# Performance work log

Measured on AMD Instinct MI355X. Metric: run time of the kernel, lower is better.

Reference implementation:

```python
import jax, jax.numpy as jnp
import numpy as np
import math

D = 2048  # hidden_size
B, S = 4, 2048
EPS = 1e-5


def _ln(z, g, b):
    m = jnp.mean(z, axis=-1, keepdims=True)
    v = jnp.mean(jnp.square(z - m), axis=-1, keepdims=True)
    return (z - m) * jax.lax.rsqrt(v + EPS) * g + b


def _rotate_half(x):
    h = x.shape[-1] // 2
    return jnp.concatenate([-x[..., h:], x[..., :h]], axis=-1)


def _mas_normalize(logits):
    m = jnp.max(jnp.abs(logits), axis=-1, keepdims=True)
    return logits / (m + 1e-9)


def setup_inputs() -> dict:
    key = jax.random.key(0)
    ks = jax.random.split(key, 12)
    std = 0.02
    return {
        "x": jax.random.normal(ks[0], (B, S, D), dtype=jnp.float32),
        "position_ids": jnp.arange(S, dtype=jnp.int32),
        "ln1_g": jnp.ones((D,), jnp.float32),
        "ln1_b": jnp.zeros((D,), jnp.float32),
        # stacked params for [q, k, v, o]
        "mu_w": std * jax.random.normal(ks[1], (4, D, D), dtype=jnp.float32),
        "mu_b": jnp.zeros((4, D), jnp.float32),
        "proto_w": std * jax.random.normal(ks[2], (4, D, D), dtype=jnp.float32),
        "gate": jnp.zeros((4, D), jnp.float32),
        "pt_w": std * jax.random.normal(ks[3], (4, D, D), dtype=jnp.float32),
        "pln_g": jnp.ones((4, D), jnp.float32),
        "pln_b": jnp.zeros((4, D), jnp.float32),
        "incoming": std * jax.random.normal(ks[4], (4, D, D), dtype=jnp.float32),
    }


def reference(x, position_ids, ln1_g, ln1_b, mu_w, mu_b, proto_w, gate,
              pt_w, pln_g, pln_b, incoming):
    d = x.shape[-1]
    inv_sqrt_d = 1.0 / math.sqrt(d)

    # proto_state = proto_weight + LN(Linear(incoming))  per module [4, D, D]
    prc = jnp.einsum('nij,noj->nio', incoming, pt_w)
    proto_state = proto_w + _ln(prc, pln_g[:, None, :], pln_b[:, None, :])

    ln1_out = _ln(x, ln1_g, ln1_b)            # [B,S,D]
    ctx = jnp.mean(ln1_out, axis=1)           # [B,D]

    # qkv computation outputs: silu(ln1_out @ mu_w.T + mu_b) for n in {q,k,v}
    comp = jax.nn.silu(jnp.einsum('bsd,nod->nbso', ln1_out, mu_w[:3])
                       + mu_b[:3][:, None, None, :])            # [3,B,S,D]
    # routing from context vector
    match_ctx = jnp.einsum('bd,nod->nbo', ctx, proto_state[:3]) * inv_sqrt_d
    routing = match_ctx + gate[:3][:, None, :]                  # [3,B,D]
    gating = _mas_normalize(routing)
    masked = gating[:, :, None, :] * comp                       # [3,B,S,D]
    q, k, v = masked[0], masked[1], masked[2]

    # RoPE over full hidden dim (num_heads == 1)
    seq = position_ids.shape[0]
    inv_freq = 1.0 / (10000.0 ** (jnp.arange(0, d, 2, dtype=jnp.float32) / d))
    t = jnp.arange(seq, dtype=jnp.float32)
    freqs = t[:, None] * inv_freq[None, :]
    emb = jnp.concatenate([freqs, freqs], axis=-1)              # [S,D]
    cos = jnp.cos(emb)[position_ids]
    sin = jnp.sin(emb)[position_ids]
    q = q * cos + _rotate_half(q) * sin
    k = k * cos + _rotate_half(k) * sin

    # causal single-head attention, scale 1/sqrt(head_dim=D)
    scores = jnp.einsum('bqd,bkd->bqk', q, k) * inv_sqrt_d      # [B,S,S]
    causal = jnp.tril(jnp.ones((seq, seq), dtype=bool))
    scores = jnp.where(causal, scores, jnp.finfo(scores.dtype).min)
    probs = jax.nn.softmax(scores, axis=-1)
    attn_out = jnp.einsum('bqk,bkd->bqd', probs, v)             # [B,S,D]

    # output SPL + routing
    ctx_o = jnp.mean(attn_out, axis=1)
    c_o = jax.nn.silu(jnp.einsum('bsd,od->bso', attn_out, mu_w[3]) + mu_b[3])
    match_o = jnp.einsum('bd,od->bo', ctx_o, proto_state[3]) * inv_sqrt_d
    gating_o = _mas_normalize(match_o + gate[3])
    x_out = x + gating_o[:, None, :] * c_o
    return x_out
```

## Files before the change

### kernel.cpp

```cpp
#include <hip/hip_runtime.h>
#include <hip/hip_bf16.h>

#define Dh 2048
#define Bh 4
#define Sh 2048
#define NROW 8192
#define HALF 1024
#define INV_SQRT_D 0.022097086912079608f
#define LNEPS 1e-5f

typedef __hip_bfloat16 bf16;
typedef short short8 __attribute__((ext_vector_type(8)));
typedef float f32x4 __attribute__((ext_vector_type(4)));

__device__ inline float warp_sum(float x) {
#pragma unroll
  for (int o = 32; o > 0; o >>= 1) x += __shfl_down(x, o);
  return x;
}
__device__ inline float warp_max(float x) {
#pragma unroll
  for (int o = 32; o > 0; o >>= 1) x = fmaxf(x, __shfl_down(x, o));
  return x;
}
__device__ inline float block_sum(float x, float* sm4) {
  x = warp_sum(x);
  int w = threadIdx.x >> 6;
  if ((threadIdx.x & 63) == 0) sm4[w] = x;
  __syncthreads();
  float r = sm4[0] + sm4[1] + sm4[2] + sm4[3];
  __syncthreads();
  return r;
}
__device__ inline float block_max(float x, float* sm4) {
  x = warp_max(x);
  int w = threadIdx.x >> 6;
  if ((threadIdx.x & 63) == 0) sm4[w] = x;
  __syncthreads();
  float r = fmaxf(fmaxf(sm4[0], sm4[1]), fmaxf(sm4[2], sm4[3]));
  __syncthreads();
  return r;
}

__device__ inline void gload_lds16(const void* g, void* lds) {
  __builtin_amdgcn_global_load_lds(
      (const __attribute__((address_space(1))) unsigned int*)(unsigned long long)g,
      (__attribute__((address_space(3))) unsigned int*)(unsigned long long)lds,
      16, 0, 0);
}

#define MM(R, AF)                                                              \
  acc[R][0] = __builtin_amdgcn_mfma_f32_16x16x32_bf16(AF, b0, acc[R][0], 0, 0, 0); \
  acc[R][1] = __builtin_amdgcn_mfma_f32_16x16x32_bf16(AF, b1, acc[R][1], 0, 0, 0); \
  acc[R][2] = __builtin_amdgcn_mfma_f32_16x16x32_bf16(AF, b2, acc[R][2], 0, 0, 0); \
  acc[R][3] = __builtin_amdgcn_mfma_f32_16x16x32_bf16(AF, b3, acc[R][3], 0, 0, 0);

template <int MODE>
__global__ __launch_bounds__(512) void pgemm(
    const bf16* __restrict__ Aall, const bf16* __restrict__ Ball,
    void* __restrict__ Call, int N, int K, int lda, int ldb,
    long sAz, long sBz, long sCz,
    const float* __restrict__ e0, const float* __restrict__ e1,
    const float* __restrict__ e2) {
  const int bm0 = blockIdx.x * 256;
  const int bn0 = blockIdx.y * 256;
  if (MODE == 2 && bn0 > bm0 + 255) return;
  const int z = blockIdx.z;
  const bf16* A = Aall + (long)z * sAz;
  const bf16* B = Ball + (long)z * sBz;

  __shared__ __align__(16) char smem[65536];
  const int tid = threadIdx.x;
  const int l = tid & 63, w = tid >> 6;
  const int wr = w >> 2, wc = w & 3;

  f32x4 acc[8][4] = {};
  const int nt = K >> 5;

  const int sg = (((l & 3) ^ ((l >> 3) & 3)) << 3);
  const int srow = (w << 4) + (l >> 2);
  const bf16* aS0 = A + (long)(bm0 + srow) * lda + sg;
  const bf16* aS1 = A + (long)(bm0 + 128 + srow) * lda + sg;
  const bf16* bS0 = B + (long)(bn0 + srow) * ldb + sg;
  const bf16* bS1 = B + (long)(bn0 + 128 + srow) * ldb + sg;
  char* const dA = smem + (w << 10);
  char* const dB = smem + 16384 + (w << 10);

  auto stageA = [&](int tt) {
    int boff = (tt & 1) << 15;
    gload_lds16(aS0 + (tt << 5), dA + boff);
    gload_lds16(aS1 + (tt << 5), dA + boff + 8192);
  };
  auto stageB = [&](int tt) {
    int boff = (tt & 1) << 15;
    gload_lds16(bS0 + (tt << 5), dB + boff);
    gload_lds16(bS1 + (tt << 5), dB + boff + 8192);
  };

  stageA(0); stageB(0);
  if (nt > 1) stageB(1);
  if (nt > 1) asm volatile("s_waitcnt vmcnt(2)" ::: "memory");
  else        asm volatile("s_waitcnt vmcnt(0)" ::: "memory");
  __builtin_amdgcn_sched_barrier(0);
  asm volatile("s_barrier" ::: "memory");

  const int rslot = (((l >> 4) ^ ((l >> 1) & 3)) << 4);
  const int abyte = (((wr << 7) + (l & 15)) << 6) + rslot;
  const int bbyte = (((wc << 6) + (l & 15)) << 6) + rslot;

  for (int t = 0; t < nt; ++t) {
    const char* Ab = smem + ((t & 1) << 15);
    const char* Bb = Ab + 16384;
    short8 b0 = *(const short8*)(Bb + bbyte);
    short8 b1 = *(const short8*)(Bb + bbyte + 1024);
    short8 b2 = *(const short8*)(Bb + bbyte + 2048);
    short8 b3 = *(const short8*)(Bb + bbyte + 3072);
    short8 a0 = *(const short8*)(Ab + abyte);
    short8 a1 = *(const short8*)(Ab + abyte + 1024);
    short8 a2 = *(const short8*)(Ab + abyte + 2048);
    short8 a3 = *(const short8*)(Ab + abyte + 3072);
    if (t + 1 < nt) stageA(t + 1);
    MM(0, a0) MM(1, a1) MM(2, a2) MM(3, a3)
    asm volatile("s_waitcnt lgkmcnt(0)" ::: "memory");
    asm volatile("s_barrier" ::: "memory");
    short8 a4 = *(const short8*)(Ab + abyte + 4096);
    short8 a5 = *(const short8*)(Ab + abyte + 5120);
    short8 a6 = *(const short8*)(Ab + abyte + 6144);
    short8 a7 = *(const short8*)(Ab + abyte + 7168);
    if (t + 2 < nt) stageB(t + 2);
    MM(4, a4) MM(5, a5) MM(6, a6) MM(7, a7)
    if (t < nt - 1) {
      asm volatile("s_waitcnt lgkmcnt(0)" ::: "memory");
      if (t + 2 < nt) asm volatile("s_waitcnt vmcnt(2)" ::: "memory");
      else            asm volatile("s_waitcnt vmcnt(0)" ::: "memory");
      __builtin_amdgcn_sched_barrier(0);
      asm volatile("s_barrier" ::: "memory");
    }
  }

  const int lc = l & 15, lr4 = (l >> 4) << 2;
#pragma unroll
  for (int fr = 0; fr < 8; ++fr) {
    int gr0 = bm0 + (wr << 7) + fr * 16 + lr4;
#pragma unroll
    for (int fc = 0; fc < 4; ++fc) {
      int gc = bn0 + (wc << 6) + fc * 16 + lc;
#pragma unroll
      for (int qv = 0; qv < 4; ++qv) {
        int gr = gr0 + qv;
        float a = acc[fr][fc][qv];
        if (MODE == 0) {
          ((float*)Call + (long)z * sCz)[(long)gr * N + gc] = a;
        } else if (MODE == 1) {
          float val = a + e0[z * Dh + gc];
          float sil = val / (1.f + __expf(-val));
          int bb = gr >> 11;
          float g = e1[(z * Bh + bb) * Dh + gc];
          ((bf16*)Call + (long)z * sCz)[(long)gr * N + gc] =
              __float2bfloat16(sil * g);
        } else if (MODE == 2) {
          ((float*)Call + (long)z * sCz)[(long)gr * N + gc] = a * INV_SQRT_D;
        } else {
          float val = a + e0[gc];
          float sil = val / (1.f + __expf(-val));
          int bb = gr >> 11;
          ((float*)Call)[(long)gr * N + gc] =
              e2[(long)gr * N + gc] + e1[bb * Dh + gc] * sil;
        }
      }
    }
  }
}

__global__ __launch_bounds__(512) void pgemm_h(
    const bf16* __restrict__ Aall, const bf16* __restrict__ Ball,
    bf16* __restrict__ Call, int N, int lda, int ldb,
    long sAz, long sBz, long sCz) {
  const int fid = blockIdx.x;
  const int p = fid >> 8, q = fid & 255;
  const int mh = q >> 5;
  const int z = (q >> 3) & 3, ni = q & 7;
  const int mi = p ? (15 - mh) : mh;
  const int bm0 = mi * 128, bn0 = ni * 256;
  const bf16* A = Aall + (long)z * sAz;
  const bf16* B = Ball + (long)z * sBz;

  __shared__ __align__(16) char smem[49152];
  const int tid = threadIdx.x;
  const int l = tid & 63, w = tid >> 6;
  const int wr = w >> 2, wc = w & 3;
  f32x4 acc[4][4] = {};
  const int nt = (bm0 + 128) >> 5;

  const int sg = (((l & 3) ^ ((l >> 3) & 3)) << 3);
  const int srow = (w << 4) + (l >> 2);
  const bf16* aS = A + (long)(bm0 + srow) * lda + sg;
  const bf16* bS0 = B + (long)(bn0 + srow) * ldb + sg;
  const bf16* bS1 = B + (long)(bn0 + 128 + srow) * ldb + sg;
  char* const dA = smem + (w << 10);
  char* const dB = smem + 8192 + (w << 10);

  auto stageA = [&](int tt) {
    gload_lds16(aS + (tt << 5), dA + (tt & 1) * 24576);
  };
  auto stageB = [&](int tt) {
    int boff = (tt & 1) * 24576;
    gload_lds16(bS0 + (tt << 5), dB + boff);
    gload_lds16(bS1 + (tt << 5), dB + boff + 8192);
  };

  stageA(0); stageB(0);
  if (nt > 1) stageB(1);
  if (nt > 1) asm volatile("s_waitcnt vmcnt(2)" ::: "memory");
  else        asm volatile("s_waitcnt vmcnt(0)" ::: "memory");
  __builtin_amdgcn_sched_barrier(0);
  asm volatile("s_barrier" ::: "memory");

  const int rslot = (((l >> 4) ^ ((l >> 1) & 3)) << 4);
  const int abyte = (((wr << 6) + (l & 15)) << 6) + rslot;
  const int bbyte = (((wc << 6) + (l & 15)) << 6) + rslot;

  for (int t = 0; t < nt; ++t) {
    const char* Ab = smem + (t & 1) * 24576;
    const char* Bb = Ab + 8192;
    short8 b0 = *(const short8*)(Bb + bbyte);
    short8 b1 = *(const short8*)(Bb + bbyte + 1024);
    short8 b2 = *(const short8*)(Bb + bbyte + 2048);
    short8 b3 = *(const short8*)(Bb + bbyte + 3072);
    short8 a0 = *(const short8*)(Ab + abyte);
    short8 a1 = *(const short8*)(Ab + abyte + 1024);
    if (t + 1 < nt) stageA(t + 1);
    MM(0, a0) MM(1, a1)
    asm volatile("s_waitcnt lgkmcnt(0)" ::: "memory");
    asm volatile("s_barrier" ::: "memory");
    short8 a2 = *(const short8*)(Ab + abyte + 2048);
    short8 a3 = *(const short8*)(Ab + abyte + 3072);
    if (t + 2 < nt) stageB(t + 2);
    MM(2, a2) MM(3, a3)
    if (t < nt - 1) {
      asm volatile("s_waitcnt lgkmcnt(0)" ::: "memory");
      if (t + 2 < nt) asm volatile("s_waitcnt vmcnt(2)" ::: "memory");
      else            asm volatile("s_waitcnt vmcnt(0)" ::: "memory");
      __builtin_amdgcn_sched_barrier(0);
      asm volatile("s_barrier" ::: "memory");
    }
  }

  const int lc = l & 15, lr4 = (l >> 4) << 2;
  bf16* C = Call + (long)z * sCz;
#pragma unroll
  for (int fr = 0; fr < 4; ++fr) {
    int gr0 = bm0 + (wr << 6) + fr * 16 + lr4;
#pragma unroll
    for (int fc = 0; fc < 4; ++fc) {
      int gc = bn0 + (wc << 6) + fc * 16 + lc;
#pragma unroll
      for (int qv = 0; qv < 4; ++qv) {
        C[(long)(gr0 + qv) * N + gc] = __float2bfloat16(acc[fr][fc][qv]);
      }
    }
  }
}

__global__ __launch_bounds__(256) void cvt3_kernel(
    const float* __restrict__ s0, const float* __restrict__ s1,
    const float* __restrict__ s2, bf16* __restrict__ o0, bf16* __restrict__ o1,
    bf16* __restrict__ o2, long n) {
  const float* in = (blockIdx.y == 0) ? s0 : (blockIdx.y == 1) ? s1 : s2;
  bf16* out = (blockIdx.y == 0) ? o0 : (blockIdx.y == 1) ? o1 : o2;
  long i = ((long)blockIdx.x * 256 + threadIdx.x) * 4;
  if (i >= n) return;
  float4 v = *(const float4*)(in + i);
  out[i + 0] = __float2bfloat16(v.x);
  out[i + 1] = __float2bfloat16(v.y);
  out[i + 2] = __float2bfloat16(v.z);
  out[i + 3] = __float2bfloat16(v.w);
}

__global__ __launch_bounds__(256) void transpose_kernel(const bf16* __restrict__ in,
                                                        bf16* __restrict__ out) {
  __shared__ bf16 t[64][65];
  int b = blockIdx.z;
  int s0 = blockIdx.x * 64, d0 = blockIdx.y * 64;
  const bf16* ib = in + (long)b * Sh * Dh;
  bf16* ob = out + (long)b * Sh * Dh;
  int tx = threadIdx.x & 63, ty = threadIdx.x >> 6;
#pragma unroll
  for (int r = ty; r < 64; r += 4) t[r][tx] = ib[(long)(s0 + r) * Dh + d0 + tx];
  __syncthreads();
#pragma unroll
  for (int r = ty; r < 64; r += 4) ob[(long)(d0 + r) * Sh + s0 + tx] = t[tx][r];
}

__global__ __launch_bounds__(256) void ln1_kernel(const float* __restrict__ x,
    const float* __restrict__ g, const float* __restrict__ b, bf16* __restrict__ out) {
  __shared__ float sm4[4];
  long r = blockIdx.x;
  const float* row = x + r * Dh;
  float v[8];
  float s = 0.f, s2 = 0.f;
#pragma unroll
  for (int c = 0; c < 8; ++c) {
    float t = row[threadIdx.x + c * 256];
    v[c] = t; s += t; s2 += t * t;
  }
  s = block_sum(s, sm4);
  s2 = block_sum(s2, sm4);
  float mean = s * (1.f / Dh);
  float rstd = rsqrtf(s2 * (1.f / Dh) - mean * mean + LNEPS);
#pragma unroll
  for (int c = 0; c < 8; ++c) {
    int o = threadIdx.x + c * 256;
    out[r * Dh + o] = __float2bfloat16((v[c] - mean) * rstd * g[o] + b[o]);
  }
}

__global__ __launch_bounds__(256) void meanrow_kernel(const bf16* __restrict__ in,
                                                      float* __restrict__ outbd) {
  int gid = blockIdx.x * 256 + threadIdx.x;
  int s0 = blockIdx.y * 128;
  long base = ((long)(gid >> 11) * Sh + s0) * Dh + (gid & 2047);
  float s = 0.f;
  for (int t = 0; t < 128; ++t) s += __bfloat162float(in[base + (long)t * Dh]);
  atomicAdd(&outbd[gid], s * (1.f / Sh));
}

__global__ __launch_bounds__(256) void route_kernel(
    const float* __restrict__ prc, const float* __restrict__ proto_w,
    const float* __restrict__ pln_g, const float* __restrict__ pln_b,
    const float* __restrict__ gate, const float* __restrict__ ctx,
    float* __restrict__ routing, float* __restrict__ ps3) {
  __shared__ float sm4[4];
  int i = blockIdx.x, n = blockIdx.y;
  long rb = ((long)n * Dh + i) * Dh;
  float v[8];
  float s = 0.f, s2 = 0.f;
#pragma unroll
  for (int c = 0; c < 8; ++c) {
    float t = prc[rb + threadIdx.x + c * 256];
    v[c] = t; s += t; s2 += t * t;
  }
  s = block_sum(s, sm4);
  s2 = block_sum(s2, sm4);
  float mean = s * (1.f / Dh);
  float rstd = rsqrtf(s2 * (1.f / Dh) - mean * mean + LNEPS);
  if (n == 3) {
#pragma unroll
    for (int c = 0; c < 8; ++c) {
      int o = threadIdx.x + c * 256;
      float ps = proto_w[rb + o] + (v[c] - mean) * rstd * pln_g[3 * Dh + o] + pln_b[3 * Dh + o];
      ps3[(long)i * Dh + o] = ps;
    }
  } else {
    float acc[4] = {0.f, 0.f, 0.f, 0.f};
#pragma unroll
    for (int c = 0; c < 8; ++c) {
      int o = threadIdx.x + c * 256;
      float ps = proto_w[rb + o] + (v[c] - mean) * rstd * pln_g[n * Dh + o] + pln_b[n * Dh + o];
#pragma unroll
      for (int b = 0; b < 4; ++b) acc[b] += ps * ctx[b * Dh + o];
    }
    for (int b = 0; b < 4; ++b) {
      float r = block_sum(acc[b], sm4);
      if (threadIdx.x == 0)
        routing[(n * 4 + b) * Dh + i] = r * INV_SQRT_D + gate[n * Dh + i];
    }
  }
}

__global__ __launch_bounds__(256) void route_o_kernel(
    const float* __restrict__ ps3, const float* __restrict__ ctxo,
    const float* __restrict__ gate, float* __restrict__ routing) {
  __shared__ float sm4[4];
  int i = blockIdx.x;
  float acc[4] = {0.f, 0.f, 0.f, 0.f};
#pragma unroll
  for (int c = 0; c < 8; ++c) {
    int o = threadIdx.x + c * 256;
    float p = ps3[(long)i * Dh + o];
#pragma unroll
    for (int b = 0; b < 4; ++b) acc[b] += p * ctxo[b * Dh + o];
  }
  for (int b = 0; b < 4; ++b) {
    float r = block_sum(acc[b], sm4);
    if (threadIdx.x == 0)
      routing[(12 + b) * Dh + i] = r * INV_SQRT_D + gate[3 * Dh + i];
  }
}

__global__ __launch_bounds__(256) void masnorm_kernel(const float* __restrict__ rin,
                                                      float* __restrict__ gout) {
  __shared__ float sm4[4];
  long r = blockIdx.x;
  float m = 0.f;
#pragma unroll
  for (int c = 0; c < 8; ++c)
    m = fmaxf(m, fabsf(rin[r * Dh + threadIdx.x + c * 256]));
  m = block_max(m, sm4);
  float inv = 1.f / (m + 1e-9f);
#pragma unroll
  for (int c = 0; c < 8; ++c) {
    int o = threadIdx.x + c * 256;
    gout[r * Dh + o] = rin[r * Dh + o] * inv;
  }
}

__global__ __launch_bounds__(256) void rope_table_kernel(float* __restrict__ cosT,
                                                         float* __restrict__ sinT) {
  int idx = blockIdx.x * 256 + threadIdx.x;
  int t = idx >> 10, f = idx & 1023;
  float inv_freq = expf(-(float)f * (9.210340371976184f / 1024.f));
  float ang = (float)t * inv_freq;
  cosT[idx] = cosf(ang);
  sinT[idx] = sinf(ang);
}

__global__ __launch_bounds__(256) void rope_kernel(bf16* __restrict__ q, bf16* __restrict__ k,
    const int* __restrict__ pos, const float* __restrict__ cosT,
    const float* __restrict__ sinT) {
  long r = blockIdx.x;
  int s = (int)(r & (Sh - 1));
  int p = pos[s];
#pragma unroll
  for (int c = 0; c < 4; ++c) {
    int t = threadIdx.x + c * 256;
    float cv = cosT[(long)p * HALF + t];
    float sv = sinT[(long)p * HALF + t];
    long i1 = r * Dh + t, i2 = i1 + HALF;
    float q1 = __bfloat162float(q[i1]), q2 = __bfloat162float(q[i2]);
    q[i1] = __float2bfloat16(q1 * cv - q2 * sv);
    q[i2] = __float2bfloat16(q2 * cv + q1 * sv);
    float k1 = __bfloat162float(k[i1]), k2 = __bfloat162float(k[i2]);
    k[i1] = __float2bfloat16(k1 * cv - k2 * sv);
    k[i2] = __float2bfloat16(k2 * cv + k1 * sv);
  }
}

__global__ __launch_bounds__(256) void softmax_kernel(const float* __restrict__ scores,
                                                      bf16* __restrict__ probs) {
  __shared__ float buf[Sh];
  __shared__ float sm4[4];
  long r = blockIdx.x;
  int qi = (int)(r & (Sh - 1));
  const float* row = scores + r * (long)Sh;
  bf16* prow = probs + r * (long)Sh;
  int n = qi + 1;
  float m = -3.0e38f;
  for (int o = threadIdx.x; o < n; o += 256) {
    float x = row[o]; buf[o] = x; m = fmaxf(m, x);
  }
  m = block_max(m, sm4);
  float s = 0.f;
  for (int o = threadIdx.x; o < n; o += 256) {
    float e = __expf(buf[o] - m); buf[o] = e; s += e;
  }
  s = block_sum(s, sm4);
  float inv = 1.f / s;
  for (int o = threadIdx.x; o < n; o += 256) prow[o] = __float2bfloat16(buf[o] * inv);
  for (int o = n + (int)threadIdx.x; o < Sh; o += 256) prow[o] = __float2bfloat16(0.f);
}

extern "C" void kernel_launch(void* const* d_in, const int* in_sizes, int n_in,
                              void* d_out, int out_size, void* d_ws, size_t ws_size,
                              hipStream_t stream) {
  const float* x       = (const float*)d_in[0];
  const int*   pos     = (const int*)d_in[1];
  const float* ln1_g   = (const float*)d_in[2];
  const float* ln1_b   = (const float*)d_in[3];
  const float* mu_w    = (const float*)d_in[4];
  const float* mu_b    = (const float*)d_in[5];
  const float* proto_w = (const float*)d_in[6];
  const float* gate    = (const float*)d_in[7];
  const float* pt_w    = (const float*)d_in[8];
  const float* pln_g   = (const float*)d_in[9];
  const float* pln_b   = (const float*)d_in[10];
  const float* incoming= (const float*)d_in[11];

  char* w = (char*)d_ws;
  const long BF = 33554432L;
  bf16*  ln1    = (bf16*)(w);
  bf16*  qb     = (bf16*)(w + BF);
  bf16*  kb     = (bf16*)(w + 2 * BF);
  bf16*  vb     = (bf16*)(w + 3 * BF);
  bf16*  attn   = (bf16*)(w + 4 * BF);
  bf16*  mu_wb  = (bf16*)(w + 5 * BF);
  bf16*  ptw_b  = (bf16*)(w + 6 * BF);
  bf16*  vT     = ptw_b;
  bf16*  inc_b  = (bf16*)(w + 7 * BF);
  bf16*  probs  = inc_b;
  float* ps3    = (float*)(w + 8 * BF);
  float* cosT   = (float*)(w + 8 * BF + 16777216L);
  float* sinT   = cosT + (long)Sh * HALF;
  float* ctx    = sinT + (long)Sh * HALF;
  float* ctxo   = ctx + Bh * Dh;
  float* routing= ctxo + Bh * Dh;
  float* gating = routing + 16 * Dh;
  float* scores = (float*)d_out;

  const long DD4 = 4L * Dh * Dh;

  hipMemsetAsync(ctx, 0, 2L * Bh * Dh * sizeof(float), stream);

  rope_table_kernel<<<(Sh * HALF) / 256, 256, 0, stream>>>(cosT, sinT);
  cvt3_kernel<<<dim3(DD4 / 1024, 3), 256, 0, stream>>>(
      mu_w, incoming, pt_w, mu_wb, inc_b, ptw_b, DD4);
  ln1_kernel<<<NROW, 256, 0, stream>>>(x, ln1_g, ln1_b, ln1);
  meanrow_kernel<<<dim3(32, 16), 256, 0, stream>>>(ln1, ctx);
  pgemm<0><<<dim3(8, 8, 4), 512, 0, stream>>>(
      inc_b, ptw_b, scores, Dh, Dh, Dh, Dh,
      (long)Dh * Dh, (long)Dh * Dh, (long)Dh * Dh, nullptr, nullptr, nullptr);
  route_kernel<<<dim3(Dh, 4), 256, 0, stream>>>(scores, proto_w, pln_g, pln_b,
                                                gate, ctx, routing, ps3);
  masnorm_kernel<<<12, 256, 0, stream>>>(routing, gating);
  pgemm<1><<<dim3(32, 8, 3), 512, 0, stream>>>(
      ln1, mu_wb, qb, Dh, Dh, Dh, Dh,
      0L, (long)Dh * Dh, (long)NROW * Dh, mu_b, gating, nullptr);
  rope_kernel<<<NROW, 256, 0, stream>>>(qb, kb, pos, cosT, sinT);
  pgemm<2><<<dim3(8, 8, 4), 512, 0, stream>>>(
      qb, kb, scores, Sh, Dh, Dh, Dh,
      (long)Sh * Dh, (long)Sh * Dh, (long)Sh * Sh, nullptr, nullptr, nullptr);
  softmax_kernel<<<Bh * Sh, 256, 0, stream>>>(scores, probs);
  transpose_kernel<<<dim3(32, 32, 4), 256, 0, stream>>>(vb, vT);
  pgemm_h<<<512, 512, 0, stream>>>(
      probs, vT, attn, Dh, Sh, Sh,
      (long)Sh * Sh, (long)Dh * Sh, (long)Sh * Dh);
  meanrow_kernel<<<dim3(32, 16), 256, 0, stream>>>(attn, ctxo);
  route_o_kernel<<<Dh, 256, 0, stream>>>(ps3, ctxo, gate, routing);
  masnorm_kernel<<<4, 256, 0, stream>>>(routing + 12 * Dh, gating + 12 * Dh);
  pgemm<4><<<dim3(32, 8, 1), 512, 0, stream>>>(
      attn, mu_wb + 3L * Dh * Dh, d_out, Dh, Dh, Dh, Dh,
      0L, 0L, 0L, mu_b + 3 * Dh, gating + 12 * Dh, x);
}
```

Before: 678.2 us.

## Fuse RoPE into QKV GEMM epilogue, load B fragments directly, store scores as fp16

The QKV GEMM epilogue now applies RoPE directly, using a column permutation so each wave holds both halves of a rotation pair, and the separate rope kernel is removed. The pgemm B operand is now read straight from global memory into registers, double-buffered across unrolled iterations instead of being staged through LDS, which halves shared memory per block. Attention scores are written and read as fp16 instead of fp32 to cut softmax input traffic. The trade-offs are uncoalesced global B loads with a full vmcnt(0) wait each tile for every GEMM mode, and reduced score precision.

```diff
diff --git a/kernel.cpp b/kernel.cpp
--- a/kernel.cpp
+++ b/kernel.cpp
@@ -1,5 +1,6 @@
 #include <hip/hip_runtime.h>
 #include <hip/hip_bf16.h>
+#include <hip/hip_fp16.h>
 
 #define Dh 2048
 #define Bh 4
@@ -50,10 +51,10 @@
 }
 
 #define MM(R, AF)                                                              \
-  acc[R][0] = __builtin_amdgcn_mfma_f32_16x16x32_bf16(AF, b0, acc[R][0], 0, 0, 0); \
-  acc[R][1] = __builtin_amdgcn_mfma_f32_16x16x32_bf16(AF, b1, acc[R][1], 0, 0, 0); \
-  acc[R][2] = __builtin_amdgcn_mfma_f32_16x16x32_bf16(AF, b2, acc[R][2], 0, 0, 0); \
-  acc[R][3] = __builtin_amdgcn_mfma_f32_16x16x32_bf16(AF, b3, acc[R][3], 0, 0, 0);
+  acc[R][0] = __builtin_amdgcn_mfma_f32_16x16x32_bf16(AF, cb0, acc[R][0], 0, 0, 0); \
+  acc[R][1] = __builtin_amdgcn_mfma_f32_16x16x32_bf16(AF, cb1, acc[R][1], 0, 0, 0); \
+  acc[R][2] = __builtin_amdgcn_mfma_f32_16x16x32_bf16(AF, cb2, acc[R][2], 0, 0, 0); \
+  acc[R][3] = __builtin_amdgcn_mfma_f32_16x16x32_bf16(AF, cb3, acc[R][3], 0, 0, 0);
 
 template <int MODE>
 __global__ __launch_bounds__(512) void pgemm(
@@ -61,15 +62,18 @@
     void* __restrict__ Call, int N, int K, int lda, int ldb,
     long sAz, long sBz, long sCz,
     const float* __restrict__ e0, const float* __restrict__ e1,
-    const float* __restrict__ e2) {
+    const float* __restrict__ e2,
+    const int* __restrict__ pos, const float* __restrict__ cosT,
+    const float* __restrict__ sinT) {
   const int bm0 = blockIdx.x * 256;
   const int bn0 = blockIdx.y * 256;
+  const int ns = blockIdx.y;
   if (MODE == 2 && bn0 > bm0 + 255) return;
   const int z = blockIdx.z;
   const bf16* A = Aall + (long)z * sAz;
   const bf16* B = Ball + (long)z * sBz;
 
-  __shared__ __align__(16) char smem[65536];
+  __shared__ __align__(16) char smem[32768];
   const int tid = threadIdx.x;
   const int l = tid & 63, w = tid >> 6;
   const int wr = w >> 2, wc = w & 3;
@@ -81,96 +85,146 @@
   const int srow = (w << 4) + (l >> 2);
   const bf16* aS0 = A + (long)(bm0 + srow) * lda + sg;
   const bf16* aS1 = A + (long)(bm0 + 128 + srow) * lda + sg;
-  const bf16* bS0 = B + (long)(bn0 + srow) * ldb + sg;
-  const bf16* bS1 = B + (long)(bn0 + 128 + srow) * ldb + sg;
   char* const dA = smem + (w << 10);
-  char* const dB = smem + 16384 + (w << 10);
-
   auto stageA = [&](int tt) {
-    int boff = (tt & 1) << 15;
+    int boff = (tt & 1) << 14;
     gload_lds16(aS0 + (tt << 5), dA + boff);
     gload_lds16(aS1 + (tt << 5), dA + boff + 8192);
   };
-  auto stageB = [&](int tt) {
-    int boff = (tt & 1) << 15;
-    gload_lds16(bS0 + (tt << 5), dB + boff);
-    gload_lds16(bS1 + (tt << 5), dB + boff + 8192);
-  };
-
-  stageA(0); stageB(0);
-  if (nt > 1) stageB(1);
-  if (nt > 1) asm volatile("s_waitcnt vmcnt(2)" ::: "memory");
-  else        asm volatile("s_waitcnt vmcnt(0)" ::: "memory");
+
+  int colb[4];
+#pragma unroll
+  for (int j = 0; j < 4; ++j) {
+    if (MODE == 1)
+      colb[j] = ((j >> 1) << 10) + (ns << 7) + (wc << 5) + ((j & 1) << 4);
+    else
+      colb[j] = bn0 + (wc << 6) + (j << 4);
+  }
+  const bf16* bP0 = B + (long)(colb[0] + (l & 15)) * ldb + ((l >> 4) << 3);
+  const bf16* bP1 = B + (long)(colb[1] + (l & 15)) * ldb + ((l >> 4) << 3);
+  const bf16* bP2 = B + (long)(colb[2] + (l & 15)) * ldb + ((l >> 4) << 3);
+  const bf16* bP3 = B + (long)(colb[3] + (l & 15)) * ldb + ((l >> 4) << 3);
+
+  short8 be0, be1, be2, be3, bo0, bo1, bo2, bo3;
+
+  stageA(0);
+  be0 = *(const short8*)(bP0);
+  be1 = *(const short8*)(bP1);
+  be2 = *(const short8*)(bP2);
+  be3 = *(const short8*)(bP3);
+  asm volatile("s_waitcnt vmcnt(0)" ::: "memory");
   __builtin_amdgcn_sched_barrier(0);
   asm volatile("s_barrier" ::: "memory");
 
   const int rslot = (((l >> 4) ^ ((l >> 1) & 3)) << 4);
   const int abyte = (((wr << 7) + (l & 15)) << 6) + rslot;
-  const int bbyte = (((wc << 6) + (l & 15)) << 6) + rslot;
-
-  for (int t = 0; t < nt; ++t) {
-    const char* Ab = smem + ((t & 1) << 15);
-    const char* Bb = Ab + 16384;
-    short8 b0 = *(const short8*)(Bb + bbyte);
-    short8 b1 = *(const short8*)(Bb + bbyte + 1024);
-    short8 b2 = *(const short8*)(Bb + bbyte + 2048);
-    short8 b3 = *(const short8*)(Bb + bbyte + 3072);
-    short8 a0 = *(const short8*)(Ab + abyte);
-    short8 a1 = *(const short8*)(Ab + abyte + 1024);
-    short8 a2 = *(const short8*)(Ab + abyte + 2048);
-    short8 a3 = *(const short8*)(Ab + abyte + 3072);
-    if (t + 1 < nt) stageA(t + 1);
-    MM(0, a0) MM(1, a1) MM(2, a2) MM(3, a3)
-    asm volatile("s_waitcnt lgkmcnt(0)" ::: "memory");
-    asm volatile("s_barrier" ::: "memory");
-    short8 a4 = *(const short8*)(Ab + abyte + 4096);
-    short8 a5 = *(const short8*)(Ab + abyte + 5120);
-    short8 a6 = *(const short8*)(Ab + abyte + 6144);
-    short8 a7 = *(const short8*)(Ab + abyte + 7168);
-    if (t + 2 < nt) stageB(t + 2);
-    MM(4, a4) MM(5, a5) MM(6, a6) MM(7, a7)
-    if (t < nt - 1) {
-      asm volatile("s_waitcnt lgkmcnt(0)" ::: "memory");
-      if (t + 2 < nt) asm volatile("s_waitcnt vmcnt(2)" ::: "memory");
-      else            asm volatile("s_waitcnt vmcnt(0)" ::: "memory");
-      __builtin_amdgcn_sched_barrier(0);
-      asm volatile("s_barrier" ::: "memory");
-    }
-  }
+
+#define TILE(T, pb0, pb1, pb2, pb3, nb0, nb1, nb2, nb3)                       \
+  {                                                                           \
+    const int t_ = (T);                                                       \
+    const char* Ab = smem + ((t_ & 1) << 14);                                 \
+    short8 cb0 = pb0, cb1 = pb1, cb2 = pb2, cb3 = pb3;                        \
+    short8 a0 = *(const short8*)(Ab + abyte);                                 \
+    short8 a1 = *(const short8*)(Ab + abyte + 1024);                          \
+    short8 a2 = *(const short8*)(Ab + abyte + 2048);                          \
+    short8 a3 = *(const short8*)(Ab + abyte + 3072);                          \
+    short8 a4 = *(const short8*)(Ab + abyte + 4096);                          \
+    short8 a5 = *(const short8*)(Ab + abyte + 5120);                          \
+    short8 a6 = *(const short8*)(Ab + abyte + 6144);                          \
+    short8 a7 = *(const short8*)(Ab + abyte + 7168);                          \
+    if (t_ + 1 < nt) {                                                        \
+      stageA(t_ + 1);                                                         \
+      nb0 = *(const short8*)(bP0 + ((t_ + 1) << 5));                          \
+      nb1 = *(const short8*)(bP1 + ((t_ + 1) << 5));                          \
+      nb2 = *(const short8*)(bP2 + ((t_ + 1) << 5));                          \
+      nb3 = *(const short8*)(bP3 + ((t_ + 1) << 5));                          \
+    }                                                                         \
+    MM(0, a0) MM(1, a1) MM(2, a2) MM(3, a3)                                   \
+    MM(4, a4) MM(5, a5) MM(6, a6) MM(7, a7)                                   \
+    if (t_ < nt - 1) {                                                        \
+      asm volatile("s_waitcnt lgkmcnt(0)" ::: "memory");                      \
+      asm volatile("s_waitcnt vmcnt(0)" ::: "memory");                        \
+      __builtin_amdgcn_sched_barrier(0);                                      \
+      asm volatile("s_barrier" ::: "memory");                                 \
+    }                                                                         \
+  }
+
+  for (int t = 0; t < nt; t += 2) {
+    TILE(t,     be0, be1, be2, be3, bo0, bo1, bo2, bo3)
+    TILE(t + 1, bo0, bo1, bo2, bo3, be0, be1, be2, be3)
+  }
+#undef TILE
 
   const int lc = l & 15, lr4 = (l >> 4) << 2;
 #pragma unroll
   for (int fr = 0; fr < 8; ++fr) {
     int gr0 = bm0 + (wr << 7) + fr * 16 + lr4;
-#pragma unroll
-    for (int fc = 0; fc < 4; ++fc) {
-      int gc = bn0 + (wc << 6) + fc * 16 + lc;
+    if (MODE == 1) {
+      int chi0 = colb[0] + lc;
 #pragma unroll
       for (int qv = 0; qv < 4; ++qv) {
         int gr = gr0 + qv;
-        float a = acc[fr][fc][qv];
-        if (MODE == 0) {
-          ((float*)Call + (long)z * sCz)[(long)gr * N + gc] = a;
-        } else if (MODE == 1) {
-          float val = a + e0[z * Dh + gc];
+        int s = gr & (Sh - 1);
+        int bb = gr >> 11;
+        float msk[4];
+#pragma unroll
+        for (int fc = 0; fc < 4; ++fc) {
+          int gc = colb[fc] + lc;
+          float val = acc[fr][fc][qv] + e0[z * Dh + gc];
           float sil = val / (1.f + __expf(-val));
-          int bb = gr >> 11;
-          float g = e1[(z * Bh + bb) * Dh + gc];
-          ((bf16*)Call + (long)z * sCz)[(long)gr * N + gc] =
-              __float2bfloat16(sil * g);
-        } else if (MODE == 2) {
-          ((float*)Call + (long)z * sCz)[(long)gr * N + gc] = a * INV_SQRT_D;
+          msk[fc] = sil * e1[(z * Bh + bb) * Dh + gc];
+        }
+        float out[4];
+        if (z < 2) {
+          int p = pos[s];
+          float cv0 = cosT[(long)p * HALF + chi0];
+          float sv0 = sinT[(long)p * HALF + chi0];
+          float cv1 = cosT[(long)p * HALF + chi0 + 16];
+          float sv1 = sinT[(long)p * HALF + chi0 + 16];
+          out[0] = msk[0] * cv0 - msk[2] * sv0;
+          out[1] = msk[1] * cv1 - msk[3] * sv1;
+          out[2] = msk[2] * cv0 + msk[0] * sv0;
+          out[3] = msk[3] * cv1 + msk[1] * sv1;
         } else {
-          float val = a + e0[gc];
-          float sil = val / (1.f + __expf(-val));
-          int bb = gr >> 11;
-          ((float*)Call)[(long)gr * N + gc] =
-              e2[(long)gr * N + gc] + e1[bb * Dh + gc] * sil;
+          out[0] = msk[0]; out[1] = msk[1]; out[2] = msk[2]; out[3] = msk[3];
+        }
+        bf16* C = (bf16*)Call + (long)z * sCz;
+#pragma unroll
+        for (int fc = 0; fc < 4; ++fc)
+          C[(long)gr * N + colb[fc] + lc] = __float2bfloat16(out[fc]);
+      }
+    } else {
+#pragma unroll
+      for (int fc = 0; fc < 4; ++fc) {
+        int gc = colb[fc] + lc;
+#pragma unroll
+        for (int qv = 0; qv < 4; ++qv) {
+          int gr = gr0 + qv;
+          float a = acc[fr][fc][qv];
+          if (MODE == 0) {
+            ((float*)Call + (long)z * sCz)[(long)gr * N + gc] = a;
+          } else if (MODE == 2) {
+            ((__half*)Call + (long)z * sCz)[(long)gr * N + gc] =
+                __float2half(a * INV_SQRT_D);
+          } else {
+            float val = a + e0[gc];
+            float sil = val / (1.f + __expf(-val));
+            int bb = gr >> 11;
+            ((float*)Call)[(long)gr * N + gc] =
+                e2[(long)gr * N + gc] + e1[bb * Dh + gc] * sil;
+          }
         }
       }
     }
   }
 }
+
+#undef MM
+#define MM(R, AF)                                                              \
+  acc[R][0] = __builtin_amdgcn_mfma_f32_16x16x32_bf16(AF, b0, acc[R][0], 0, 0, 0); \
+  acc[R][1] = __builtin_amdgcn_mfma_f32_16x16x32_bf16(AF, b1, acc[R][1], 0, 0, 0); \
+  acc[R][2] = __builtin_amdgcn_mfma_f32_16x16x32_bf16(AF, b2, acc[R][2], 0, 0, 0); \
+  acc[R][3] = __builtin_amdgcn_mfma_f32_16x16x32_bf16(AF, b3, acc[R][3], 0, 0, 0);
 
 __global__ __launch_bounds__(512) void pgemm_h(
     const bf16* __restrict__ Aall, const bf16* __restrict__ Ball,
@@ -194,7 +248,7 @@
 
   const int sg = (((l & 3) ^ ((l >> 3) & 3)) << 3);
   const int srow = (w << 4) + (l >> 2);
-  const bf16* aS = A + (long)(bm0 + srow) * lda + sg;
+  const bf16* aS  = A + (long)(bm0 + srow) * lda + sg;
   const bf16* bS0 = B + (long)(bn0 + srow) * ldb + sg;
   const bf16* bS1 = B + (long)(bn0 + 128 + srow) * ldb + sg;
   char* const dA = smem + (w << 10);
@@ -255,9 +309,8 @@
     for (int fc = 0; fc < 4; ++fc) {
       int gc = bn0 + (wc << 6) + fc * 16 + lc;
 #pragma unroll
-      for (int qv = 0; qv < 4; ++qv) {
+      for (int qv = 0; qv < 4; ++qv)
         C[(long)(gr0 + qv) * N + gc] = __float2bfloat16(acc[fr][fc][qv]);
-      }
     }
   }
 }
@@ -415,39 +468,18 @@
   sinT[idx] = sinf(ang);
 }
 
-__global__ __launch_bounds__(256) void rope_kernel(bf16* __restrict__ q, bf16* __restrict__ k,
-    const int* __restrict__ pos, const float* __restrict__ cosT,
-    const float* __restrict__ sinT) {
-  long r = blockIdx.x;
-  int s = (int)(r & (Sh - 1));
-  int p = pos[s];
-#pragma unroll
-  for (int c = 0; c < 4; ++c) {
-    int t = threadIdx.x + c * 256;
-    float cv = cosT[(long)p * HALF + t];
-    float sv = sinT[(long)p * HALF + t];
-    long i1 = r * Dh + t, i2 = i1 + HALF;
-    float q1 = __bfloat162float(q[i1]), q2 = __bfloat162float(q[i2]);
-    q[i1] = __float2bfloat16(q1 * cv - q2 * sv);
-    q[i2] = __float2bfloat16(q2 * cv + q1 * sv);
-    float k1 = __bfloat162float(k[i1]), k2 = __bfloat162float(k[i2]);
-    k[i1] = __float2bfloat16(k1 * cv - k2 * sv);
-    k[i2] = __float2bfloat16(k2 * cv + k1 * sv);
-  }
-}
-
-__global__ __launch_bounds__(256) void softmax_kernel(const float* __restrict__ scores,
+__global__ __launch_bounds__(256) void softmax_kernel(const __half* __restrict__ scores,
                                                       bf16* __restrict__ probs) {
   __shared__ float buf[Sh];
   __shared__ float sm4[4];
   long r = blockIdx.x;
   int qi = (int)(r & (Sh - 1));
-  const float* row = scores + r * (long)Sh;
+  const __half* row = scores + r * (long)Sh;
   bf16* prow = probs + r * (long)Sh;
   int n = qi + 1;
   float m = -3.0e38f;
   for (int o = threadIdx.x; o < n; o += 256) {
-    float x = row[o]; buf[o] = x; m = fmaxf(m, x);
+    float x = __half2float(row[o]); buf[o] = x; m = fmaxf(m, x);
   }
   m = block_max(m, sm4);
   float s = 0.f;
@@ -495,7 +527,8 @@
   float* ctxo   = ctx + Bh * Dh;
   float* routing= ctxo + Bh * Dh;
   float* gating = routing + 16 * Dh;
-  float* scores = (float*)d_out;
+  float*  prc    = (float*)d_out;
+  __half* scores = (__half*)d_out;
 
   const long DD4 = 4L * Dh * Dh;
 
@@ -507,18 +540,20 @@
   ln1_kernel<<<NROW, 256, 0, stream>>>(x, ln1_g, ln1_b, ln1);
   meanrow_kernel<<<dim3(32, 16), 256, 0, stream>>>(ln1, ctx);
   pgemm<0><<<dim3(8, 8, 4), 512, 0, stream>>>(
-      inc_b, ptw_b, scores, Dh, Dh, Dh, Dh,
-      (long)Dh * Dh, (long)Dh * Dh, (long)Dh * Dh, nullptr, nullptr, nullptr);
-  route_kernel<<<dim3(Dh, 4), 256, 0, stream>>>(scores, proto_w, pln_g, pln_b,
+      inc_b, ptw_b, prc, Dh, Dh, Dh, Dh,
+      (long)Dh * Dh, (long)Dh * Dh, (long)Dh * Dh,
+      nullptr, nullptr, nullptr, nullptr, nullptr, nullptr);
+  route_kernel<<<dim3(Dh, 4), 256, 0, stream>>>(prc, proto_w, pln_g, pln_b,
                                                 gate, ctx, routing, ps3);
   masnorm_kernel<<<12, 256, 0, stream>>>(routing, gating);
   pgemm<1><<<dim3(32, 8, 3), 512, 0, stream>>>(
       ln1, mu_wb, qb, Dh, Dh, Dh, Dh,
-      0L, (long)Dh * Dh, (long)NROW * Dh, mu_b, gating, nullptr);
-  rope_kernel<<<NROW, 256, 0, stream>>>(qb, kb, pos, cosT, sinT);
+      0L, (long)Dh * Dh, (long)NROW * Dh, mu_b, gating, nullptr,
+      pos, cosT, sinT);
   pgemm<2><<<dim3(8, 8, 4), 512, 0, stream>>>(
       qb, kb, scores, Sh, Dh, Dh, Dh,
-      (long)Sh * Dh, (long)Sh * Dh, (long)Sh * Sh, nullptr, nullptr, nullptr);
+      (long)Sh * Dh, (long)Sh * Dh, (long)Sh * Sh,
+      nullptr, nullptr, nullptr, nullptr, nullptr, nullptr);
   softmax_kernel<<<Bh * Sh, 256, 0, stream>>>(scores, probs);
   transpose_kernel<<<dim3(32, 32, 4), 256, 0, stream>>>(vb, vT);
   pgemm_h<<<512, 512, 0, stream>>>(
@@ -529,5 +564,6 @@
   masnorm_kernel<<<4, 256, 0, stream>>>(routing + 12 * Dh, gating + 12 * Dh);
   pgemm<4><<<dim3(32, 8, 1), 512, 0, stream>>>(
       attn, mu_wb + 3L * Dh * Dh, d_out, Dh, Dh, Dh, Dh,
-      0L, 0L, 0L, mu_b + 3 * Dh, gating + 12 * Dh, x);
-}
+      0L, 0L, 0L, mu_b + 3 * Dh, gating + 12 * Dh, x,
+      nullptr, nullptr, nullptr);
+}
```

Result: slower. 934.8 us (+37.8%).

## Fuse RoPE into QKV GEMM epilogue and store attention scores as fp16

Applied to the files above, without the earlier changes.

The QKV GEMM now remaps its B-tile rows so each block holds matching column pairs i and i+1024. That lets the epilogue apply the rotary embedding directly, and the separate rope_kernel pass over q and k is removed. The QK^T GEMM also writes scores as fp16 instead of fp32, which halves the score write and read traffic for softmax. The costs are scattered B-row loads in the QKV GEMM and reduced score precision, which risks overflow or precision loss in fp16.

```diff
diff --git a/kernel.cpp b/kernel.cpp
--- a/kernel.cpp
+++ b/kernel.cpp
@@ -1,5 +1,6 @@
 #include <hip/hip_runtime.h>
 #include <hip/hip_bf16.h>
+#include <hip/hip_fp16.h>
 
 #define Dh 2048
 #define Bh 4
@@ -61,9 +62,12 @@
     void* __restrict__ Call, int N, int K, int lda, int ldb,
     long sAz, long sBz, long sCz,
     const float* __restrict__ e0, const float* __restrict__ e1,
-    const float* __restrict__ e2) {
+    const float* __restrict__ e2,
+    const int* __restrict__ pos, const float* __restrict__ cosT,
+    const float* __restrict__ sinT) {
   const int bm0 = blockIdx.x * 256;
   const int bn0 = blockIdx.y * 256;
+  const int ns = blockIdx.y;
   if (MODE == 2 && bn0 > bm0 + 255) return;
   const int z = blockIdx.z;
   const bf16* A = Aall + (long)z * sAz;
@@ -81,8 +85,16 @@
   const int srow = (w << 4) + (l >> 2);
   const bf16* aS0 = A + (long)(bm0 + srow) * lda + sg;
   const bf16* aS1 = A + (long)(bm0 + 128 + srow) * lda + sg;
-  const bf16* bS0 = B + (long)(bn0 + srow) * ldb + sg;
-  const bf16* bS1 = B + (long)(bn0 + 128 + srow) * ldb + sg;
+  auto bmap = [&](int r) -> const bf16* {
+    if (MODE == 1) {
+      int wcr = r >> 6, fcr = (r >> 4) & 3, ir = r & 15;
+      int g = ((fcr >> 1) << 10) + (ns << 7) + (wcr << 5) + ((fcr & 1) << 4) + ir;
+      return B + (long)g * ldb + sg;
+    }
+    return B + (long)(bn0 + r) * ldb + sg;
+  };
+  const bf16* bS0 = bmap(srow);
+  const bf16* bS1 = bmap(128 + srow);
   char* const dA = smem + (w << 10);
   char* const dB = smem + 16384 + (w << 10);
 
@@ -142,30 +154,64 @@
 #pragma unroll
   for (int fr = 0; fr < 8; ++fr) {
     int gr0 = bm0 + (wr << 7) + fr * 16 + lr4;
-#pragma unroll
-    for (int fc = 0; fc < 4; ++fc) {
-      int gc = bn0 + (wc << 6) + fc * 16 + lc;
+    if (MODE == 1) {
+      int colb[4];
+#pragma unroll
+      for (int fc = 0; fc < 4; ++fc)
+        colb[fc] = ((fc >> 1) << 10) + (ns << 7) + (wc << 5) + ((fc & 1) << 4);
+      int chi0 = (ns << 7) + (wc << 5) + lc;
 #pragma unroll
       for (int qv = 0; qv < 4; ++qv) {
         int gr = gr0 + qv;
-        float a = acc[fr][fc][qv];
-        if (MODE == 0) {
-          ((float*)Call + (long)z * sCz)[(long)gr * N + gc] = a;
-        } else if (MODE == 1) {
-          float val = a + e0[z * Dh + gc];
+        int s = gr & (Sh - 1);
+        int bb = gr >> 11;
+        float msk[4];
+#pragma unroll
+        for (int fc = 0; fc < 4; ++fc) {
+          int gc = colb[fc] + lc;
+          float val = acc[fr][fc][qv] + e0[z * Dh + gc];
           float sil = val / (1.f + __expf(-val));
-          int bb = gr >> 11;
-          float g = e1[(z * Bh + bb) * Dh + gc];
-          ((bf16*)Call + (long)z * sCz)[(long)gr * N + gc] =
-              __float2bfloat16(sil * g);
-        } else if (MODE == 2) {
-          ((float*)Call + (long)z * sCz)[(long)gr * N + gc] = a * INV_SQRT_D;
+          msk[fc] = sil * e1[(z * Bh + bb) * Dh + gc];
+        }
+        float out[4];
+        if (z < 2) {
+          int p = pos[s];
+          float cv0 = cosT[(long)p * HALF + chi0];
+          float sv0 = sinT[(long)p * HALF + chi0];
+          float cv1 = cosT[(long)p * HALF + chi0 + 16];
+          float sv1 = sinT[(long)p * HALF + chi0 + 16];
+          out[0] = msk[0] * cv0 - msk[2] * sv0;
+          out[1] = msk[1] * cv1 - msk[3] * sv1;
+          out[2] = msk[2] * cv0 + msk[0] * sv0;
+          out[3] = msk[3] * cv1 + msk[1] * sv1;
         } else {
-          float val = a + e0[gc];
-          float sil = val / (1.f + __expf(-val));
-          int bb = gr >> 11;
-          ((float*)Call)[(long)gr * N + gc] =
-              e2[(long)gr * N + gc] + e1[bb * Dh + gc] * sil;
+          out[0] = msk[0]; out[1] = msk[1]; out[2] = msk[2]; out[3] = msk[3];
+        }
+        bf16* C = (bf16*)Call + (long)z * sCz;
+#pragma unroll
+        for (int fc = 0; fc < 4; ++fc)
+          C[(long)gr * N + colb[fc] + lc] = __float2bfloat16(out[fc]);
+      }
+    } else {
+#pragma unroll
+      for (int fc = 0; fc < 4; ++fc) {
+        int gc = bn0 + (wc << 6) + fc * 16 + lc;
+#pragma unroll
+        for (int qv = 0; qv < 4; ++qv) {
+          int gr = gr0 + qv;
+          float a = acc[fr][fc][qv];
+          if (MODE == 0) {
+            ((float*)Call + (long)z * sCz)[(long)gr * N + gc] = a;
+          } else if (MODE == 2) {
+            ((__half*)Call + (long)z * sCz)[(long)gr * N + gc] =
+                __float2half(a * INV_SQRT_D);
+          } else {
+            float val = a + e0[gc];
+            float sil = val / (1.f + __expf(-val));
+            int bb = gr >> 11;
+            ((float*)Call)[(long)gr * N + gc] =
+                e2[(long)gr * N + gc] + e1[bb * Dh + gc] * sil;
+          }
         }
       }
     }
@@ -194,7 +240,7 @@
 
   const int sg = (((l & 3) ^ ((l >> 3) & 3)) << 3);
   const int srow = (w << 4) + (l >> 2);
-  const bf16* aS = A + (long)(bm0 + srow) * lda + sg;
+  const bf16* aS  = A + (long)(bm0 + srow) * lda + sg;
   const bf16* bS0 = B + (long)(bn0 + srow) * ldb + sg;
   const bf16* bS1 = B + (long)(bn0 + 128 + srow) * ldb + sg;
   char* const dA = smem + (w << 10);
@@ -255,9 +301,8 @@
     for (int fc = 0; fc < 4; ++fc) {
       int gc = bn0 + (wc << 6) + fc * 16 + lc;
 #pragma unroll
-      for (int qv = 0; qv < 4; ++qv) {
+      for (int qv = 0; qv < 4; ++qv)
         C[(long)(gr0 + qv) * N + gc] = __float2bfloat16(acc[fr][fc][qv]);
-      }
     }
   }
 }
@@ -415,39 +460,18 @@
   sinT[idx] = sinf(ang);
 }
 
-__global__ __launch_bounds__(256) void rope_kernel(bf16* __restrict__ q, bf16* __restrict__ k,
-    const int* __restrict__ pos, const float* __restrict__ cosT,
-    const float* __restrict__ sinT) {
-  long r = blockIdx.x;
-  int s = (int)(r & (Sh - 1));
-  int p = pos[s];
-#pragma unroll
-  for (int c = 0; c < 4; ++c) {
-    int t = threadIdx.x + c * 256;
-    float cv = cosT[(long)p * HALF + t];
-    float sv = sinT[(long)p * HALF + t];
-    long i1 = r * Dh + t, i2 = i1 + HALF;
-    float q1 = __bfloat162float(q[i1]), q2 = __bfloat162float(q[i2]);
-    q[i1] = __float2bfloat16(q1 * cv - q2 * sv);
-    q[i2] = __float2bfloat16(q2 * cv + q1 * sv);
-    float k1 = __bfloat162float(k[i1]), k2 = __bfloat162float(k[i2]);
-    k[i1] = __float2bfloat16(k1 * cv - k2 * sv);
-    k[i2] = __float2bfloat16(k2 * cv + k1 * sv);
-  }
-}
-
-__global__ __launch_bounds__(256) void softmax_kernel(const float* __restrict__ scores,
+__global__ __launch_bounds__(256) void softmax_kernel(const __half* __restrict__ scores,
                                                       bf16* __restrict__ probs) {
   __shared__ float buf[Sh];
   __shared__ float sm4[4];
   long r = blockIdx.x;
   int qi = (int)(r & (Sh - 1));
-  const float* row = scores + r * (long)Sh;
+  const __half* row = scores + r * (long)Sh;
   bf16* prow = probs + r * (long)Sh;
   int n = qi + 1;
   float m = -3.0e38f;
   for (int o = threadIdx.x; o < n; o += 256) {
-    float x = row[o]; buf[o] = x; m = fmaxf(m, x);
+    float x = __half2float(row[o]); buf[o] = x; m = fmaxf(m, x);
   }
   m = block_max(m, sm4);
   float s = 0.f;
@@ -495,7 +519,8 @@
   float* ctxo   = ctx + Bh * Dh;
   float* routing= ctxo + Bh * Dh;
   float* gating = routing + 16 * Dh;
-  float* scores = (float*)d_out;
+  float*  prc    = (float*)d_out;
+  __half* scores = (__half*)d_out;
 
   const long DD4 = 4L * Dh * Dh;
 
@@ -507,18 +532,20 @@
   ln1_kernel<<<NROW, 256, 0, stream>>>(x, ln1_g, ln1_b, ln1);
   meanrow_kernel<<<dim3(32, 16), 256, 0, stream>>>(ln1, ctx);
   pgemm<0><<<dim3(8, 8, 4), 512, 0, stream>>>(
-      inc_b, ptw_b, scores, Dh, Dh, Dh, Dh,
-      (long)Dh * Dh, (long)Dh * Dh, (long)Dh * Dh, nullptr, nullptr, nullptr);
-  route_kernel<<<dim3(Dh, 4), 256, 0, stream>>>(scores, proto_w, pln_g, pln_b,
+      inc_b, ptw_b, prc, Dh, Dh, Dh, Dh,
+      (long)Dh * Dh, (long)Dh * Dh, (long)Dh * Dh,
+      nullptr, nullptr, nullptr, nullptr, nullptr, nullptr);
+  route_kernel<<<dim3(Dh, 4), 256, 0, stream>>>(prc, proto_w, pln_g, pln_b,
                                                 gate, ctx, routing, ps3);
   masnorm_kernel<<<12, 256, 0, stream>>>(routing, gating);
   pgemm<1><<<dim3(32, 8, 3), 512, 0, stream>>>(
       ln1, mu_wb, qb, Dh, Dh, Dh, Dh,
-      0L, (long)Dh * Dh, (long)NROW * Dh, mu_b, gating, nullptr);
-  rope_kernel<<<NROW, 256, 0, stream>>>(qb, kb, pos, cosT, sinT);
+      0L, (long)Dh * Dh, (long)NROW * Dh, mu_b, gating, nullptr,
+      pos, cosT, sinT);
   pgemm<2><<<dim3(8, 8, 4), 512, 0, stream>>>(
       qb, kb, scores, Sh, Dh, Dh, Dh,
-      (long)Sh * Dh, (long)Sh * Dh, (long)Sh * Sh, nullptr, nullptr, nullptr);
+      (long)Sh * Dh, (long)Sh * Dh, (long)Sh * Sh,
+      nullptr, nullptr, nullptr, nullptr, nullptr, nullptr);
   softmax_kernel<<<Bh * Sh, 256, 0, stream>>>(scores, probs);
   transpose_kernel<<<dim3(32, 32, 4), 256, 0, stream>>>(vb, vT);
   pgemm_h<<<512, 512, 0, stream>>>(
@@ -529,5 +556,6 @@
   masnorm_kernel<<<4, 256, 0, stream>>>(routing + 12 * Dh, gating + 12 * Dh);
   pgemm<4><<<dim3(32, 8, 1), 512, 0, stream>>>(
       attn, mu_wb + 3L * Dh * Dh, d_out, Dh, Dh, Dh, Dh,
-      0L, 0L, 0L, mu_b + 3 * Dh, gating + 12 * Dh, x);
-}
+      0L, 0L, 0L, mu_b + 3 * Dh, gating + 12 * Dh, x,
+      nullptr, nullptr, nullptr);
+}
```

After: 669.7 us. Within noise of the previous version (-1.3%).
